# Optimization experiments

Measured on AMD Instinct MI355X. Metric: run time of the kernel, lower is better.

Reference implementation:

```python
import jax, jax.numpy as jnp
import numpy as np

N, C, H, W = 64, 128, 32, 32
EPS = 1e-5


def _layernorm_chw(x, w, b):
    # LayerNorm over normalized_shape=(C,H,W): last 3 dims
    mu = jnp.mean(x, axis=(1, 2, 3), keepdims=True)
    var = jnp.var(x, axis=(1, 2, 3), keepdims=True)
    return (x - mu) * jax.lax.rsqrt(var + EPS) * w[None] + b[None]


def _conv1x1(x, w, b):
    # x: [N,C,H,W], w: [Cout,Cin], b: [Cout]
    return jnp.einsum('oc,nchw->nohw', w, x) + b[None, :, None, None]


def setup_inputs() -> dict:
    key = jax.random.key(0)
    ks = jax.random.split(key, 12)
    d = {
        'query': jax.random.normal(ks[0], (N, C, H, W), jnp.float32),
        'key': jax.random.normal(ks[1], (N, C, H, W), jnp.float32),
        'value': jax.random.normal(ks[2], (N, C, H, W), jnp.float32),
        'ln1_w': jnp.ones((C, H, W), jnp.float32),
        'ln1_b': jnp.zeros((C, H, W), jnp.float32),
        'ln2_w': jnp.ones((C, H, W), jnp.float32),
        'ln2_b': jnp.zeros((C, H, W), jnp.float32),
        'ln3_w': jnp.ones((C, H, W), jnp.float32),
        'ln3_b': jnp.zeros((C, H, W), jnp.float32),
        'wq': jax.random.normal(ks[3], (C, C), jnp.float32) / np.sqrt(C),
        'bq': jnp.zeros((C,), jnp.float32),
        'wk': jax.random.normal(ks[4], (C, C), jnp.float32) / np.sqrt(C),
        'bk': jnp.zeros((C,), jnp.float32),
        'wv': jax.random.normal(ks[5], (C, C), jnp.float32) / np.sqrt(C),
        'bv': jnp.zeros((C,), jnp.float32),
    }
    return d


def reference(query, key, value, ln1_w, ln1_b, ln2_w, ln2_b, ln3_w, ln3_b,
              wq, bq, wk, bk, wv, bv):
    qn = _layernorm_chw(query, ln1_w, ln1_b)  # residual uses normalized query
    kn = _layernorm_chw(key, ln2_w, ln2_b)
    vn = _layernorm_chw(value, ln3_w, ln3_b)
    q = _conv1x1(qn, wq, bq).reshape(N, C, H * W)
    k = _conv1x1(kn, wk, bk).reshape(N, C, H * W)
    v = _conv1x1(vn, wv, bv).reshape(N, C, H * W)
    # attention[n,i,j] = sum_c k[n,c,i] q[n,c,j] / sqrt(C); softmax over i (dim=1)
    attn = jnp.einsum('nci,ncj->nij', k, q) / jnp.sqrt(jnp.float32(C))
    attn = jax.nn.softmax(attn, axis=1)
    out = jnp.einsum('nci,nij->ncj', v, attn).reshape(N, C, H, W)
    x = qn + out
    return x.reshape(N, -1)  # flatten(start_dim=1)
```

## Files before the change

kernel.cpp:

```cpp
#include <hip/hip_runtime.h>


#define NS 64
#define CD 128
#define SD 1024
#define MEL (CD*SD)
#define SCALE 0.08838834764831845f

typedef __attribute__((ext_vector_type(4))) float floatx4;
typedef __attribute__((ext_vector_type(8))) short short8;
typedef __attribute__((ext_vector_type(4))) short short4v;

typedef __attribute__((address_space(1))) const void global_cvoid;
typedef __attribute__((address_space(3))) void lds_void;

__device__ __forceinline__ void gl16(const void* g, void* l) {
  __builtin_amdgcn_global_load_lds((global_cvoid*)g, (lds_void*)l, 16, 0, 0);
}
__device__ __forceinline__ unsigned short f2bf(float f) {
  union { float f; unsigned int i; } v; v.f = f;
  unsigned int i = v.i;
  return (unsigned short)((i + 0x7fffu + ((i >> 16) & 1u)) >> 16);
}
__device__ __forceinline__ short8 ld8_bf16(const float* __restrict__ p) {
  floatx4 a = *(const floatx4*)p;
  floatx4 b = *(const floatx4*)(p + 4);
  short8 r;
  r[0] = (short)f2bf(a[0]); r[1] = (short)f2bf(a[1]);
  r[2] = (short)f2bf(a[2]); r[3] = (short)f2bf(a[3]);
  r[4] = (short)f2bf(b[0]); r[5] = (short)f2bf(b[1]);
  r[6] = (short)f2bf(b[2]); r[7] = (short)f2bf(b[3]);
  return r;
}
__device__ __forceinline__ floatx4 mfma16(short8 a, short8 b, floatx4 c) {
  return __builtin_amdgcn_mfma_f32_16x16x32_bf16(a, b, c, 0, 0, 0);
}

__global__ __launch_bounds__(512) void stats_kernel(
    const float* __restrict__ q, const float* __restrict__ k,
    const float* __restrict__ v, float* __restrict__ sums)
{
  int tn = blockIdx.x;
  int t = tn >> 6;
  const float* x = (t == 0 ? q : (t == 1 ? k : v)) + (size_t)(tn & 63) * MEL;
  float s1 = 0.f, s2 = 0.f;
  for (int it = 0; it < 64; ++it) {
    floatx4 u = *(const floatx4*)(x + it * 2048 + threadIdx.x * 4);
#pragma unroll
    for (int j = 0; j < 4; ++j) { float f = u[j]; s1 += f; s2 += f * f; }
  }
#pragma unroll
  for (int off = 32; off; off >>= 1) {
    s1 += __shfl_xor(s1, off, 64);
    s2 += __shfl_xor(s2, off, 64);
  }
  __shared__ float r1[8], r2[8];
  int w = threadIdx.x >> 6;
  if ((threadIdx.x & 63) == 0) { r1[w] = s1; r2[w] = s2; }
  __syncthreads();
  if (threadIdx.x == 0) {
    float a = 0.f, b = 0.f;
#pragma unroll
    for (int i = 0; i < 8; ++i) { a += r1[i]; b += r2[i]; }
    sums[tn] = a; sums[192 + tn] = b;
  }
}

__global__ __launch_bounds__(512, 4) void proj_kernel(
  const float* __restrict__ k, const float* __restrict__ v,
  const float* __restrict__ l2w, const float* __restrict__ l2b,
  const float* __restrict__ l3w, const float* __restrict__ l3b,
  const float* __restrict__ wk, const float* __restrict__ bk,
  const float* __restrict__ wv, const float* __restrict__ bv,
  const float* __restrict__ sums,
  unsigned short* __restrict__ kT, unsigned short* __restrict__ vN)
{
  int n  = blockIdx.x, t = blockIdx.y, st = blockIdx.z;
  const float* x  = (t == 0 ? k : v) + (size_t)n * MEL;
  const float* lw = (t == 0 ? l2w : l3w);
  const float* lb = (t == 0 ? l2b : l3b);
  const float* W  = (t == 0 ? wk : wv);
  const float* Bs = (t == 0 ? bk : bv);

  float mu  = sums[(t + 1) * 64 + n] * (1.f / MEL);
  float var = sums[192 + (t + 1) * 64 + n] * (1.f / MEL) - mu * mu;
  float rs  = rsqrtf(var + 1e-5f);
  float a_ln = rs, b_ln = -mu * rs;

  __shared__ __align__(16) unsigned short Xt[128 * 136];

  int tid = threadIdx.x;
  int cb = tid & 15, sb = (tid >> 4) & 15, half = tid >> 8;
  int s0 = st * 128;

  unsigned int w32[8][2];
#pragma unroll
  for (int pr = 0; pr < 2; ++pr) {
    int c0 = cb * 8 + half * 4 + pr * 2;
    const float* xp0 = x  + (size_t)c0 * SD + s0 + sb * 8;
    const float* wp0 = lw + (size_t)c0 * SD + s0 + sb * 8;
    const float* bp0 = lb + (size_t)c0 * SD + s0 + sb * 8;
    float xv0[8], xv1[8], wv0[8], wv1[8], bv0[8], bv1[8];
    *(floatx4*)xv0 = *(const floatx4*)xp0;       *(floatx4*)(xv0+4) = *(const floatx4*)(xp0+4);
    *(floatx4*)xv1 = *(const floatx4*)(xp0+SD);  *(floatx4*)(xv1+4) = *(const floatx4*)(xp0+SD+4);
    *(floatx4*)wv0 = *(const floatx4*)wp0;       *(floatx4*)(wv0+4) = *(const floatx4*)(wp0+4);
    *(floatx4*)wv1 = *(const floatx4*)(wp0+SD);  *(floatx4*)(wv1+4) = *(const floatx4*)(wp0+SD+4);
    *(floatx4*)bv0 = *(const floatx4*)bp0;       *(floatx4*)(bv0+4) = *(const floatx4*)(bp0+4);
    *(floatx4*)bv1 = *(const floatx4*)(bp0+SD);  *(floatx4*)(bv1+4) = *(const floatx4*)(bp0+SD+4);
#pragma unroll
    for (int js = 0; js < 8; ++js) {
      unsigned int lo = f2bf((xv0[js] * a_ln + b_ln) * wv0[js] + bv0[js]);
      unsigned int hi = f2bf((xv1[js] * a_ln + b_ln) * wv1[js] + bv1[js]);
      w32[js][pr] = lo | (hi << 16);
    }
  }
#pragma unroll
  for (int js = 0; js < 8; ++js) {
    unsigned int* d = (unsigned int*)&Xt[(sb * 8 + js) * 136 + cb * 8 + half * 4];
    d[0] = w32[js][0]; d[1] = w32[js][1];
  }
  __syncthreads();

  int lane = tid & 63, w = tid >> 6;
  int quad = lane >> 4, l16 = lane & 15;

  short8 Af[4];
#pragma unroll
  for (int kk = 0; kk < 4; ++kk)
    Af[kk] = ld8_bf16(W + (w * 16 + l16) * CD + kk * 32 + quad * 8);

  floatx4 acc[8];
  floatx4 zz = {0.f, 0.f, 0.f, 0.f};
#pragma unroll
  for (int nb = 0; nb < 8; ++nb) acc[nb] = zz;
#pragma unroll
  for (int kk = 0; kk < 4; ++kk)
#pragma unroll
    for (int nb = 0; nb < 8; ++nb) {
      short8 Bf = *(const short8*)&Xt[(nb * 16 + l16) * 136 + kk * 32 + quad * 8];
      acc[nb] = mfma16(Af[kk], Bf, acc[nb]);
    }

  float bsv[4];
#pragma unroll
  for (int r = 0; r < 4; ++r) bsv[r] = Bs[w * 16 + quad * 4 + r];

  if (t == 0) {
#pragma unroll
    for (int nb = 0; nb < 8; ++nb) {
      short4v pk;
#pragma unroll
      for (int r = 0; r < 4; ++r) pk[r] = (short)f2bf(acc[nb][r] + bsv[r]);
      size_t g = (size_t)n * MEL + (size_t)(s0 + nb * 16 + l16) * CD + w * 16 + quad * 4;
      *(short4v*)(kT + g) = pk;
    }
  } else {
#pragma unroll
    for (int nb = 0; nb < 8; ++nb)
#pragma unroll
      for (int r = 0; r < 4; ++r) {
        size_t g = (size_t)n * MEL + (size_t)(w * 16 + quad * 4 + r) * SD + s0 + nb * 16 + l16;
        vN[g] = f2bf(acc[nb][r] + bsv[r]);
      }
  }
}

__global__ __launch_bounds__(256, 2) void attn_kernel(
  const float* __restrict__ qraw, const float* __restrict__ l1w,
  const float* __restrict__ l1b, const float* __restrict__ wq,
  const float* __restrict__ bq,
  const unsigned short* __restrict__ kT, const unsigned short* __restrict__ vN,
  const float* __restrict__ sums, float* __restrict__ out)
{
  int n = blockIdx.x, jt = blockIdx.y;
  int j0 = jt * 128;

  __shared__ __align__(16) char smem[51712];
  unsigned short* Xt = (unsigned short*)smem;
  unsigned short* Ks = (unsigned short*)smem;
  unsigned short* Vs = (unsigned short*)(smem + 16384);
  unsigned short* Ps = (unsigned short*)(smem + 34816);
  float* l_s = (float*)(smem + 51200);

  int tid = threadIdx.x, lane = tid & 63, w = tid >> 6;
  int quad = lane >> 4, l16 = lane & 15;

  float mu  = sums[n] * (1.f / MEL);
  float var = sums[192 + n] * (1.f / MEL) - mu * mu;
  float rsd = rsqrtf(var + 1e-5f);
  float a_ln = rsd, b_ln = -mu * rsd;
  const float* qb = qraw + (size_t)n * MEL;

  {
    int cb = tid & 15, sb = tid >> 4;
    unsigned int w32[8][4];
#pragma unroll
    for (int pr = 0; pr < 4; ++pr) {
      int c0 = cb * 8 + pr * 2;
      const float* xp0 = qb  + (size_t)c0 * SD + j0 + sb * 8;
      const float* wp0 = l1w + (size_t)c0 * SD + j0 + sb * 8;
      const float* bp0 = l1b + (size_t)c0 * SD + j0 + sb * 8;
      float xv0[8], xv1[8], wv0[8], wv1[8], bv0[8], bv1[8];
      *(floatx4*)xv0 = *(const floatx4*)xp0;       *(floatx4*)(xv0+4) = *(const floatx4*)(xp0+4);
      *(floatx4*)xv1 = *(const floatx4*)(xp0+SD);  *(floatx4*)(xv1+4) = *(const floatx4*)(xp0+SD+4);
      *(floatx4*)wv0 = *(const floatx4*)wp0;       *(floatx4*)(wv0+4) = *(const floatx4*)(wp0+4);
      *(floatx4*)wv1 = *(const floatx4*)(wp0+SD);  *(floatx4*)(wv1+4) = *(const floatx4*)(wp0+SD+4);
      *(floatx4*)bv0 = *(const floatx4*)bp0;       *(floatx4*)(bv0+4) = *(const floatx4*)(bp0+4);
      *(floatx4*)bv1 = *(const floatx4*)(bp0+SD);  *(floatx4*)(bv1+4) = *(const floatx4*)(bp0+SD+4);
#pragma unroll
      for (int js = 0; js < 8; ++js) {
        unsigned int lo = f2bf((xv0[js] * a_ln + b_ln) * wv0[js] + bv0[js]);
        unsigned int hi = f2bf((xv1[js] * a_ln + b_ln) * wv1[js] + bv1[js]);
        w32[js][pr] = lo | (hi << 16);
      }
    }
#pragma unroll
    for (int js = 0; js < 8; ++js)
      *(floatx4*)&Xt[(sb * 8 + js) * 136 + cb * 8] = *(floatx4*)w32[js];
  }
  __syncthreads();

  floatx4 zz = {0.f, 0.f, 0.f, 0.f};
  {
    short8 Af[2][4];
#pragma unroll
    for (int mi = 0; mi < 2; ++mi)
#pragma unroll
      for (int kk = 0; kk < 4; ++kk)
        Af[mi][kk] = ld8_bf16(wq + ((w * 2 + mi) * 16 + l16) * CD + kk * 32 + quad * 8);
    floatx4 accq[2][8];
#pragma unroll
    for (int mi = 0; mi < 2; ++mi)
#pragma unroll
      for (int nb = 0; nb < 8; ++nb) accq[mi][nb] = zz;
#pragma unroll
    for (int kk = 0; kk < 4; ++kk)
#pragma unroll
      for (int nb = 0; nb < 8; ++nb) {
        short8 Bf = *(const short8*)&Xt[(nb * 16 + l16) * 136 + kk * 32 + quad * 8];
        accq[0][nb] = mfma16(Af[0][kk], Bf, accq[0][nb]);
        accq[1][nb] = mfma16(Af[1][kk], Bf, accq[1][nb]);
      }
    __syncthreads();
    float bqs[2][4];
#pragma unroll
    for (int mi = 0; mi < 2; ++mi)
#pragma unroll
      for (int r = 0; r < 4; ++r) bqs[mi][r] = bq[(w * 2 + mi) * 16 + quad * 4 + r];
#pragma unroll
    for (int mi = 0; mi < 2; ++mi)
#pragma unroll
      for (int nb = 0; nb < 8; ++nb) {
        short4v pk;
#pragma unroll
        for (int r = 0; r < 4; ++r) pk[r] = (short)f2bf(accq[mi][nb][r] + bqs[mi][r]);
        *(short4v*)&Xt[(nb * 16 + l16) * 136 + (w * 2 + mi) * 16 + quad * 4] = pk;
      }
  }
  __syncthreads();

  short8 Qf[2][4];
#pragma unroll
  for (int nt = 0; nt < 2; ++nt)
#pragma unroll
    for (int kk = 0; kk < 4; ++kk)
      Qf[nt][kk] = *(const short8*)&Xt[((w * 2 + nt) * 16 + l16) * 136 + kk * 32 + quad * 8];
  __syncthreads();

  floatx4 Oc[2][8];
#pragma unroll
  for (int mi = 0; mi < 2; ++mi)
#pragma unroll
    for (int nb = 0; nb < 8; ++nb) Oc[mi][nb] = zz;
  float lsum[2] = {0.f, 0.f};

  const unsigned short* kbase0 = kT + (size_t)n * MEL;
  const unsigned short* vbase0 = vN + (size_t)n * MEL;

  for (int itile = 0; itile < 16; ++itile) {
    int i0 = itile * 64;
    const unsigned short* kbase = kbase0 + (size_t)i0 * CD;
#pragma unroll
    for (int it = 0; it < 4; ++it) {
      int nch = w * 256 + it * 64 + lane;
      int i = nch >> 4, cc = nch & 15;
      int csrc = (cc & 8) | ((cc & 7) ^ (i & 7));
      gl16(kbase + i * CD + csrc * 8, (char*)Ks + (w * 256 + it * 64) * 16);
    }
#pragma unroll
    for (int it = 0; it < 4; ++it) {
      int nch = w * 256 + it * 64 + lane;
      int c = nch >> 3, ci = nch & 7;
      int isrc = ci ^ (c & 7);
      gl16(vbase0 + (size_t)c * SD + i0 + isrc * 8, (char*)Vs + (w * 256 + it * 64) * 16);
    }
    __syncthreads();

    floatx4 Sa[4][2];
#pragma unroll
    for (int mt = 0; mt < 4; ++mt) { Sa[mt][0] = zz; Sa[mt][1] = zz; }
#pragma unroll
    for (int kk = 0; kk < 4; ++kk)
#pragma unroll
      for (int mt = 0; mt < 4; ++mt) {
        short8 Kf = *(const short8*)&Ks[(mt * 16 + l16) * 128 + (((kk * 4 + quad) ^ (l16 & 7)) * 8)];
        Sa[mt][0] = mfma16(Kf, Qf[0][kk], Sa[mt][0]);
        Sa[mt][1] = mfma16(Kf, Qf[1][kk], Sa[mt][1]);
      }

#pragma unroll
    for (int nt = 0; nt < 2; ++nt) {
      int jrow = (w * 2 + nt) * 16 + l16;
      int rowbase = jrow * 64;
      int sub = (quad & 1) * 4;
#pragma unroll
      for (int mt = 0; mt < 4; ++mt) {
        float p0 = __expf(Sa[mt][nt][0] * SCALE);
        float p1 = __expf(Sa[mt][nt][1] * SCALE);
        float p2 = __expf(Sa[mt][nt][2] * SCALE);
        float p3 = __expf(Sa[mt][nt][3] * SCALE);
        lsum[nt] += (p0 + p1) + (p2 + p3);
        short4v pk;
        pk[0] = (short)f2bf(p0); pk[1] = (short)f2bf(p1);
        pk[2] = (short)f2bf(p2); pk[3] = (short)f2bf(p3);
        int ci = mt * 2 + (quad >> 1);
        int cis = ci ^ (l16 & 7);
        *(short4v*)&Ps[rowbase + cis * 8 + sub] = pk;
      }
    }
    __syncthreads();

#pragma unroll
    for (int kk = 0; kk < 2; ++kk) {
      short8 Vf[2];
#pragma unroll
      for (int mi = 0; mi < 2; ++mi) {
        int c = (w * 2 + mi) * 16 + l16;
        Vf[mi] = *(const short8*)&Vs[c * 64 + (((kk * 4 + quad) ^ (l16 & 7)) * 8)];
      }
#pragma unroll
      for (int nb = 0; nb < 8; ++nb) {
        short8 Pf = *(const short8*)&Ps[(nb * 16 + l16) * 64 + (((kk * 4 + quad) ^ (l16 & 7)) * 8)];
        Oc[0][nb] = mfma16(Vf[0], Pf, Oc[0][nb]);
        Oc[1][nb] = mfma16(Vf[1], Pf, Oc[1][nb]);
      }
    }
    __syncthreads();
  }

#pragma unroll
  for (int nt = 0; nt < 2; ++nt) {
    lsum[nt] += __shfl_xor(lsum[nt], 16, 64);
    lsum[nt] += __shfl_xor(lsum[nt], 32, 64);
  }
  if (lane < 16) { l_s[(w * 2) * 16 + l16] = lsum[0]; l_s[(w * 2 + 1) * 16 + l16] = lsum[1]; }
  __syncthreads();

  float linv[8];
#pragma unroll
  for (int nb = 0; nb < 8; ++nb) linv[nb] = 1.f / l_s[nb * 16 + l16];
#pragma unroll
  for (int mi = 0; mi < 2; ++mi) {
#pragma unroll
    for (int r = 0; r < 4; ++r) {
      int c = (w * 2 + mi) * 16 + quad * 4 + r;
      const float* qp = qb  + (size_t)c * SD + j0;
      const float* wp = l1w + (size_t)c * SD + j0;
      const float* bp = l1b + (size_t)c * SD + j0;
      float* op = out + (size_t)n * MEL + (size_t)c * SD + j0;
#pragma unroll
      for (int nb = 0; nb < 8; ++nb) {
        int j = nb * 16 + l16;
        float qn = (qp[j] * a_ln + b_ln) * wp[j] + bp[j];
        op[j] = Oc[mi][nb][r] * linv[nb] + qn;
      }
    }
  }
}

extern "C" void kernel_launch(void* const* d_in, const int* in_sizes, int n_in,
                              void* d_out, int out_size, void* d_ws, size_t ws_size,
                              hipStream_t stream)
{
  const float* q   = (const float*)d_in[0];
  const float* k   = (const float*)d_in[1];
  const float* v   = (const float*)d_in[2];
  const float* l1w = (const float*)d_in[3];
  const float* l1b = (const float*)d_in[4];
  const float* l2w = (const float*)d_in[5];
  const float* l2b = (const float*)d_in[6];
  const float* l3w = (const float*)d_in[7];
  const float* l3b = (const float*)d_in[8];
  const float* wq  = (const float*)d_in[9];
  const float* bq  = (const float*)d_in[10];
  const float* wk  = (const float*)d_in[11];
  const float* bk  = (const float*)d_in[12];
  const float* wv  = (const float*)d_in[13];
  const float* bv  = (const float*)d_in[14];

  char* ws = (char*)d_ws;
  float* sums = (float*)ws;
  unsigned short* kT = (unsigned short*)(ws + 4096);
  unsigned short* vN = kT + (size_t)NS * MEL;

  stats_kernel<<<192, 512, 0, stream>>>(q, k, v, sums);
  proj_kernel<<<dim3(64, 2, 8), 512, 0, stream>>>(k, v, l2w, l2b, l3w, l3b,
      wk, bk, wv, bv, sums, kT, vN);
  attn_kernel<<<dim3(64, 8), 256, 0, stream>>>(q, l1w, l1b, wq, bq, kT, vN,
      sums, (float*)d_out);
}
```

Measured before the change: 253.6 us.

## Split stats reduction, stage projection outputs in LDS, widen attention blocks to 512 threads

The stats kernel now splits each sample's reduction into two halves across a second grid dimension, doubling the block count. The projection kernel switches to XOR-swizzled LDS without padding and stages K/V outputs in LDS so they can be written as coalesced 16-byte stores, where V previously used scattered 2-byte stores. The attention kernel goes from 256 to 512 threads with a smaller LDS footprint, splits S and O tiles across more waves, and reuses the K buffer for P. The cost is extra syncs and combining partial softmax sums through LDS.

```diff
diff --git a/kernel.cpp b/kernel.cpp
--- a/kernel.cpp
+++ b/kernel.cpp
@@ -41,10 +41,12 @@
     const float* __restrict__ v, float* __restrict__ sums)
 {
   int tn = blockIdx.x;
+  int part = blockIdx.y;
   int t = tn >> 6;
-  const float* x = (t == 0 ? q : (t == 1 ? k : v)) + (size_t)(tn & 63) * MEL;
+  const float* x = (t == 0 ? q : (t == 1 ? k : v)) + (size_t)(tn & 63) * MEL
+                   + part * (MEL / 2);
   float s1 = 0.f, s2 = 0.f;
-  for (int it = 0; it < 64; ++it) {
+  for (int it = 0; it < 32; ++it) {
     floatx4 u = *(const floatx4*)(x + it * 2048 + threadIdx.x * 4);
 #pragma unroll
     for (int j = 0; j < 4; ++j) { float f = u[j]; s1 += f; s2 += f * f; }
@@ -62,7 +64,7 @@
     float a = 0.f, b = 0.f;
 #pragma unroll
     for (int i = 0; i < 8; ++i) { a += r1[i]; b += r2[i]; }
-    sums[tn] = a; sums[192 + tn] = b;
+    sums[part * 192 + tn] = a; sums[384 + part * 192 + tn] = b;
   }
 }
 
@@ -82,12 +84,15 @@
   const float* W  = (t == 0 ? wk : wv);
   const float* Bs = (t == 0 ? bk : bv);
 
-  float mu  = sums[(t + 1) * 64 + n] * (1.f / MEL);
-  float var = sums[192 + (t + 1) * 64 + n] * (1.f / MEL) - mu * mu;
+  int si = (t + 1) * 64 + n;
+  float s1 = sums[si] + sums[192 + si];
+  float s2 = sums[384 + si] + sums[576 + si];
+  float mu  = s1 * (1.f / MEL);
+  float var = s2 * (1.f / MEL) - mu * mu;
   float rs  = rsqrtf(var + 1e-5f);
   float a_ln = rs, b_ln = -mu * rs;
 
-  __shared__ __align__(16) unsigned short Xt[128 * 136];
+  __shared__ __align__(16) unsigned short Xt[128 * 128];
 
   int tid = threadIdx.x;
   int cb = tid & 15, sb = (tid >> 4) & 15, half = tid >> 8;
@@ -116,7 +121,7 @@
   }
 #pragma unroll
   for (int js = 0; js < 8; ++js) {
-    unsigned int* d = (unsigned int*)&Xt[(sb * 8 + js) * 136 + cb * 8 + half * 4];
+    unsigned int* d = (unsigned int*)&Xt[(sb * 8 + js) * 128 + ((cb ^ js) * 8) + half * 4];
     d[0] = w32[js][0]; d[1] = w32[js][1];
   }
   __syncthreads();
@@ -124,48 +129,67 @@
   int lane = tid & 63, w = tid >> 6;
   int quad = lane >> 4, l16 = lane & 15;
 
-  short8 Af[4];
+  short8 Wf[4];
 #pragma unroll
   for (int kk = 0; kk < 4; ++kk)
-    Af[kk] = ld8_bf16(W + (w * 16 + l16) * CD + kk * 32 + quad * 8);
+    Wf[kk] = ld8_bf16(W + (w * 16 + l16) * CD + kk * 32 + quad * 8);
 
   floatx4 acc[8];
   floatx4 zz = {0.f, 0.f, 0.f, 0.f};
 #pragma unroll
-  for (int nb = 0; nb < 8; ++nb) acc[nb] = zz;
+  for (int sblk = 0; sblk < 8; ++sblk) acc[sblk] = zz;
 #pragma unroll
   for (int kk = 0; kk < 4; ++kk)
 #pragma unroll
-    for (int nb = 0; nb < 8; ++nb) {
-      short8 Bf = *(const short8*)&Xt[(nb * 16 + l16) * 136 + kk * 32 + quad * 8];
-      acc[nb] = mfma16(Af[kk], Bf, acc[nb]);
-    }
-
-  float bsv[4];
-#pragma unroll
-  for (int r = 0; r < 4; ++r) bsv[r] = Bs[w * 16 + quad * 4 + r];
+    for (int sblk = 0; sblk < 8; ++sblk) {
+      short8 Xf = *(const short8*)&Xt[(sblk * 16 + l16) * 128 +
+                                      (((kk * 4 + quad) ^ (l16 & 7)) * 8)];
+      acc[sblk] = (t == 0) ? mfma16(Wf[kk], Xf, acc[sblk])
+                           : mfma16(Xf, Wf[kk], acc[sblk]);
+    }
+  __syncthreads();
 
   if (t == 0) {
-#pragma unroll
-    for (int nb = 0; nb < 8; ++nb) {
+    float bsv[4];
+#pragma unroll
+    for (int r = 0; r < 4; ++r) bsv[r] = Bs[w * 16 + quad * 4 + r];
+#pragma unroll
+    for (int sblk = 0; sblk < 8; ++sblk) {
       short4v pk;
 #pragma unroll
-      for (int r = 0; r < 4; ++r) pk[r] = (short)f2bf(acc[nb][r] + bsv[r]);
-      size_t g = (size_t)n * MEL + (size_t)(s0 + nb * 16 + l16) * CD + w * 16 + quad * 4;
-      *(short4v*)(kT + g) = pk;
+      for (int r = 0; r < 4; ++r) pk[r] = (short)f2bf(acc[sblk][r] + bsv[r]);
+      int row = sblk * 16 + l16;
+      int cblk = w * 2 + (quad >> 1);
+      *(short4v*)&Xt[row * 128 + ((cblk ^ (l16 & 7)) * 8) + (quad & 1) * 4] = pk;
     }
   } else {
-#pragma unroll
-    for (int nb = 0; nb < 8; ++nb)
-#pragma unroll
-      for (int r = 0; r < 4; ++r) {
-        size_t g = (size_t)n * MEL + (size_t)(w * 16 + quad * 4 + r) * SD + s0 + nb * 16 + l16;
-        vN[g] = f2bf(acc[nb][r] + bsv[r]);
-      }
-  }
-}
-
-__global__ __launch_bounds__(256, 2) void attn_kernel(
+    float bsv = Bs[w * 16 + l16];
+#pragma unroll
+    for (int sblk = 0; sblk < 8; ++sblk) {
+      short4v pk;
+#pragma unroll
+      for (int r = 0; r < 4; ++r) pk[r] = (short)f2bf(acc[sblk][r] + bsv);
+      int row = w * 16 + l16;
+      int cblk = sblk * 2 + (quad >> 1);
+      *(short4v*)&Xt[row * 128 + ((cblk ^ (l16 & 7)) * 8) + (quad & 1) * 4] = pk;
+    }
+  }
+  __syncthreads();
+
+  unsigned short* outp = (t == 0 ? kT : vN);
+#pragma unroll
+  for (int it = 0; it < 4; ++it) {
+    int id = it * 512 + tid;
+    int row = id >> 4, ch = id & 15;
+    short8 u = *(const short8*)&Xt[row * 128 + ((ch ^ (row & 7)) * 8)];
+    size_t g;
+    if (t == 0) g = (size_t)n * MEL + (size_t)(s0 + row) * CD + ch * 8;
+    else        g = (size_t)n * MEL + (size_t)row * SD + s0 + ch * 8;
+    *(short8*)(outp + g) = u;
+  }
+}
+
+__global__ __launch_bounds__(512, 4) void attn_kernel(
   const float* __restrict__ qraw, const float* __restrict__ l1w,
   const float* __restrict__ l1b, const float* __restrict__ wq,
   const float* __restrict__ bq,
@@ -175,28 +199,30 @@
   int n = blockIdx.x, jt = blockIdx.y;
   int j0 = jt * 128;
 
-  __shared__ __align__(16) char smem[51712];
+  __shared__ __align__(16) char smem[33792];
   unsigned short* Xt = (unsigned short*)smem;
   unsigned short* Ks = (unsigned short*)smem;
+  unsigned short* Ps = (unsigned short*)smem;
   unsigned short* Vs = (unsigned short*)(smem + 16384);
-  unsigned short* Ps = (unsigned short*)(smem + 34816);
-  float* l_s = (float*)(smem + 51200);
+  float* l_part = (float*)(smem + 32768);
 
   int tid = threadIdx.x, lane = tid & 63, w = tid >> 6;
   int quad = lane >> 4, l16 = lane & 15;
 
-  float mu  = sums[n] * (1.f / MEL);
-  float var = sums[192 + n] * (1.f / MEL) - mu * mu;
+  float s1 = sums[n] + sums[192 + n];
+  float s2 = sums[384 + n] + sums[576 + n];
+  float mu  = s1 * (1.f / MEL);
+  float var = s2 * (1.f / MEL) - mu * mu;
   float rsd = rsqrtf(var + 1e-5f);
   float a_ln = rsd, b_ln = -mu * rsd;
   const float* qb = qraw + (size_t)n * MEL;
 
   {
-    int cb = tid & 15, sb = tid >> 4;
-    unsigned int w32[8][4];
-#pragma unroll
-    for (int pr = 0; pr < 4; ++pr) {
-      int c0 = cb * 8 + pr * 2;
+    int cb = tid & 15, sb = (tid >> 4) & 15, half = tid >> 8;
+    unsigned int w32[8][2];
+#pragma unroll
+    for (int pr = 0; pr < 2; ++pr) {
+      int c0 = cb * 8 + half * 4 + pr * 2;
       const float* xp0 = qb  + (size_t)c0 * SD + j0 + sb * 8;
       const float* wp0 = l1w + (size_t)c0 * SD + j0 + sb * 8;
       const float* bp0 = l1b + (size_t)c0 * SD + j0 + sb * 8;
@@ -215,63 +241,61 @@
       }
     }
 #pragma unroll
-    for (int js = 0; js < 8; ++js)
-      *(floatx4*)&Xt[(sb * 8 + js) * 136 + cb * 8] = *(floatx4*)w32[js];
+    for (int js = 0; js < 8; ++js) {
+      unsigned int* d = (unsigned int*)&Xt[(sb * 8 + js) * 128 + ((cb ^ js) * 8) + half * 4];
+      d[0] = w32[js][0]; d[1] = w32[js][1];
+    }
   }
   __syncthreads();
 
   floatx4 zz = {0.f, 0.f, 0.f, 0.f};
   {
-    short8 Af[2][4];
-#pragma unroll
-    for (int mi = 0; mi < 2; ++mi)
-#pragma unroll
-      for (int kk = 0; kk < 4; ++kk)
-        Af[mi][kk] = ld8_bf16(wq + ((w * 2 + mi) * 16 + l16) * CD + kk * 32 + quad * 8);
-    floatx4 accq[2][8];
-#pragma unroll
-    for (int mi = 0; mi < 2; ++mi)
-#pragma unroll
-      for (int nb = 0; nb < 8; ++nb) accq[mi][nb] = zz;
+    short8 Wf[4];
 #pragma unroll
     for (int kk = 0; kk < 4; ++kk)
+      Wf[kk] = ld8_bf16(wq + (w * 16 + l16) * CD + kk * 32 + quad * 8);
+    floatx4 accq[8];
+#pragma unroll
+    for (int nb = 0; nb < 8; ++nb) accq[nb] = zz;
+#pragma unroll
+    for (int kk = 0; kk < 4; ++kk)
 #pragma unroll
       for (int nb = 0; nb < 8; ++nb) {
-        short8 Bf = *(const short8*)&Xt[(nb * 16 + l16) * 136 + kk * 32 + quad * 8];
-        accq[0][nb] = mfma16(Af[0][kk], Bf, accq[0][nb]);
-        accq[1][nb] = mfma16(Af[1][kk], Bf, accq[1][nb]);
+        short8 Bf = *(const short8*)&Xt[(nb * 16 + l16) * 128 +
+                                        (((kk * 4 + quad) ^ (l16 & 7)) * 8)];
+        accq[nb] = mfma16(Wf[kk], Bf, accq[nb]);
       }
     __syncthreads();
-    float bqs[2][4];
-#pragma unroll
-    for (int mi = 0; mi < 2; ++mi)
-#pragma unroll
-      for (int r = 0; r < 4; ++r) bqs[mi][r] = bq[(w * 2 + mi) * 16 + quad * 4 + r];
-#pragma unroll
-    for (int mi = 0; mi < 2; ++mi)
-#pragma unroll
-      for (int nb = 0; nb < 8; ++nb) {
-        short4v pk;
-#pragma unroll
-        for (int r = 0; r < 4; ++r) pk[r] = (short)f2bf(accq[mi][nb][r] + bqs[mi][r]);
-        *(short4v*)&Xt[(nb * 16 + l16) * 136 + (w * 2 + mi) * 16 + quad * 4] = pk;
-      }
+    float bqs[4];
+#pragma unroll
+    for (int r = 0; r < 4; ++r) bqs[r] = bq[w * 16 + quad * 4 + r];
+#pragma unroll
+    for (int nb = 0; nb < 8; ++nb) {
+      short4v pk;
+#pragma unroll
+      for (int r = 0; r < 4; ++r) pk[r] = (short)f2bf(accq[nb][r] + bqs[r]);
+      int row = nb * 16 + l16;
+      int cblk = w * 2 + (quad >> 1);
+      *(short4v*)&Xt[row * 128 + ((cblk ^ (l16 & 7)) * 8) + (quad & 1) * 4] = pk;
+    }
   }
   __syncthreads();
 
   short8 Qf[2][4];
 #pragma unroll
-  for (int nt = 0; nt < 2; ++nt)
+  for (int ntl = 0; ntl < 2; ++ntl) {
+    int row = ((w >> 1) * 2 + ntl) * 16 + l16;
 #pragma unroll
     for (int kk = 0; kk < 4; ++kk)
-      Qf[nt][kk] = *(const short8*)&Xt[((w * 2 + nt) * 16 + l16) * 136 + kk * 32 + quad * 8];
-  __syncthreads();
-
-  floatx4 Oc[2][8];
+      Qf[ntl][kk] = *(const short8*)&Xt[row * 128 + (((kk * 4 + quad) ^ (l16 & 7)) * 8)];
+  }
+  __syncthreads();
+
+  floatx4 Oc[2][4];
 #pragma unroll
   for (int mi = 0; mi < 2; ++mi)
 #pragma unroll
-    for (int nb = 0; nb < 8; ++nb) Oc[mi][nb] = zz;
+    for (int nb = 0; nb < 4; ++nb) Oc[mi][nb] = zz;
   float lsum[2] = {0.f, 0.f};
 
   const unsigned short* kbase0 = kT + (size_t)n * MEL;
@@ -281,51 +305,56 @@
     int i0 = itile * 64;
     const unsigned short* kbase = kbase0 + (size_t)i0 * CD;
 #pragma unroll
-    for (int it = 0; it < 4; ++it) {
-      int nch = w * 256 + it * 64 + lane;
+    for (int it = 0; it < 2; ++it) {
+      int nch = it * 512 + tid;
       int i = nch >> 4, cc = nch & 15;
       int csrc = (cc & 8) | ((cc & 7) ^ (i & 7));
-      gl16(kbase + i * CD + csrc * 8, (char*)Ks + (w * 256 + it * 64) * 16);
-    }
-#pragma unroll
-    for (int it = 0; it < 4; ++it) {
-      int nch = w * 256 + it * 64 + lane;
+      gl16(kbase + i * CD + csrc * 8, Ks + nch * 8);
+    }
+#pragma unroll
+    for (int it = 0; it < 2; ++it) {
+      int nch = it * 512 + tid;
       int c = nch >> 3, ci = nch & 7;
       int isrc = ci ^ (c & 7);
-      gl16(vbase0 + (size_t)c * SD + i0 + isrc * 8, (char*)Vs + (w * 256 + it * 64) * 16);
+      gl16(vbase0 + (size_t)c * SD + i0 + isrc * 8, Vs + nch * 8);
     }
     __syncthreads();
 
-    floatx4 Sa[4][2];
-#pragma unroll
-    for (int mt = 0; mt < 4; ++mt) { Sa[mt][0] = zz; Sa[mt][1] = zz; }
-#pragma unroll
-    for (int kk = 0; kk < 4; ++kk)
-#pragma unroll
-      for (int mt = 0; mt < 4; ++mt) {
-        short8 Kf = *(const short8*)&Ks[(mt * 16 + l16) * 128 + (((kk * 4 + quad) ^ (l16 & 7)) * 8)];
-        Sa[mt][0] = mfma16(Kf, Qf[0][kk], Sa[mt][0]);
-        Sa[mt][1] = mfma16(Kf, Qf[1][kk], Sa[mt][1]);
-      }
-
-#pragma unroll
-    for (int nt = 0; nt < 2; ++nt) {
-      int jrow = (w * 2 + nt) * 16 + l16;
-      int rowbase = jrow * 64;
-      int sub = (quad & 1) * 4;
-#pragma unroll
-      for (int mt = 0; mt < 4; ++mt) {
-        float p0 = __expf(Sa[mt][nt][0] * SCALE);
-        float p1 = __expf(Sa[mt][nt][1] * SCALE);
-        float p2 = __expf(Sa[mt][nt][2] * SCALE);
-        float p3 = __expf(Sa[mt][nt][3] * SCALE);
-        lsum[nt] += (p0 + p1) + (p2 + p3);
+    floatx4 Sa[2][2];
+#pragma unroll
+    for (int a = 0; a < 2; ++a) { Sa[a][0] = zz; Sa[a][1] = zz; }
+#pragma unroll
+    for (int kk = 0; kk < 4; ++kk) {
+      short8 Kf[2];
+#pragma unroll
+      for (int mtl = 0; mtl < 2; ++mtl) {
+        int row = ((w & 1) * 2 + mtl) * 16 + l16;
+        Kf[mtl] = *(const short8*)&Ks[row * 128 + (((kk * 4 + quad) ^ (l16 & 7)) * 8)];
+      }
+#pragma unroll
+      for (int mtl = 0; mtl < 2; ++mtl)
+#pragma unroll
+        for (int ntl = 0; ntl < 2; ++ntl)
+          Sa[mtl][ntl] = mfma16(Kf[mtl], Qf[ntl][kk], Sa[mtl][ntl]);
+    }
+    __syncthreads();
+
+#pragma unroll
+    for (int mtl = 0; mtl < 2; ++mtl) {
+      int mt = (w & 1) * 2 + mtl;
+#pragma unroll
+      for (int ntl = 0; ntl < 2; ++ntl) {
+        float p0 = __expf(Sa[mtl][ntl][0] * SCALE);
+        float p1 = __expf(Sa[mtl][ntl][1] * SCALE);
+        float p2 = __expf(Sa[mtl][ntl][2] * SCALE);
+        float p3 = __expf(Sa[mtl][ntl][3] * SCALE);
+        lsum[ntl] += (p0 + p1) + (p2 + p3);
         short4v pk;
         pk[0] = (short)f2bf(p0); pk[1] = (short)f2bf(p1);
         pk[2] = (short)f2bf(p2); pk[3] = (short)f2bf(p3);
-        int ci = mt * 2 + (quad >> 1);
-        int cis = ci ^ (l16 & 7);
-        *(short4v*)&Ps[rowbase + cis * 8 + sub] = pk;
+        int jrow = ((w >> 1) * 2 + ntl) * 16 + l16;
+        int cis = (mt * 2 + (quad >> 1)) ^ (l16 & 7);
+        *(short4v*)&Ps[jrow * 64 + cis * 8 + (quad & 1) * 4] = pk;
       }
     }
     __syncthreads();
@@ -335,12 +364,13 @@
       short8 Vf[2];
 #pragma unroll
       for (int mi = 0; mi < 2; ++mi) {
-        int c = (w * 2 + mi) * 16 + l16;
+        int c = ((w & 3) * 2 + mi) * 16 + l16;
         Vf[mi] = *(const short8*)&Vs[c * 64 + (((kk * 4 + quad) ^ (l16 & 7)) * 8)];
       }
 #pragma unroll
-      for (int nb = 0; nb < 8; ++nb) {
-        short8 Pf = *(const short8*)&Ps[(nb * 16 + l16) * 64 + (((kk * 4 + quad) ^ (l16 & 7)) * 8)];
+      for (int nb = 0; nb < 4; ++nb) {
+        int j = ((w >> 2) * 4 + nb) * 16 + l16;
+        short8 Pf = *(const short8*)&Ps[j * 64 + (((kk * 4 + quad) ^ (l16 & 7)) * 8)];
         Oc[0][nb] = mfma16(Vf[0], Pf, Oc[0][nb]);
         Oc[1][nb] = mfma16(Vf[1], Pf, Oc[1][nb]);
       }
@@ -349,28 +379,35 @@
   }
 
 #pragma unroll
-  for (int nt = 0; nt < 2; ++nt) {
-    lsum[nt] += __shfl_xor(lsum[nt], 16, 64);
-    lsum[nt] += __shfl_xor(lsum[nt], 32, 64);
-  }
-  if (lane < 16) { l_s[(w * 2) * 16 + l16] = lsum[0]; l_s[(w * 2 + 1) * 16 + l16] = lsum[1]; }
-  __syncthreads();
-
-  float linv[8];
-#pragma unroll
-  for (int nb = 0; nb < 8; ++nb) linv[nb] = 1.f / l_s[nb * 16 + l16];
+  for (int ntl = 0; ntl < 2; ++ntl) {
+    lsum[ntl] += __shfl_xor(lsum[ntl], 16, 64);
+    lsum[ntl] += __shfl_xor(lsum[ntl], 32, 64);
+  }
+  if (lane < 16) {
+#pragma unroll
+    for (int ntl = 0; ntl < 2; ++ntl)
+      l_part[(w & 1) * 128 + ((w >> 1) * 2 + ntl) * 16 + lane] = lsum[ntl];
+  }
+  __syncthreads();
+
+  float linv[4];
+#pragma unroll
+  for (int nb = 0; nb < 4; ++nb) {
+    int j = ((w >> 2) * 4 + nb) * 16 + l16;
+    linv[nb] = 1.f / (l_part[j] + l_part[128 + j]);
+  }
 #pragma unroll
   for (int mi = 0; mi < 2; ++mi) {
 #pragma unroll
     for (int r = 0; r < 4; ++r) {
-      int c = (w * 2 + mi) * 16 + quad * 4 + r;
+      int c = ((w & 3) * 2 + mi) * 16 + quad * 4 + r;
       const float* qp = qb  + (size_t)c * SD + j0;
       const float* wp = l1w + (size_t)c * SD + j0;
       const float* bp = l1b + (size_t)c * SD + j0;
       float* op = out + (size_t)n * MEL + (size_t)c * SD + j0;
 #pragma unroll
-      for (int nb = 0; nb < 8; ++nb) {
-        int j = nb * 16 + l16;
+      for (int nb = 0; nb < 4; ++nb) {
+        int j = ((w >> 2) * 4 + nb) * 16 + l16;
         float qn = (qp[j] * a_ln + b_ln) * wp[j] + bp[j];
         op[j] = Oc[mi][nb][r] * linv[nb] + qn;
       }
@@ -403,9 +440,9 @@
   unsigned short* kT = (unsigned short*)(ws + 4096);
   unsigned short* vN = kT + (size_t)NS * MEL;
 
-  stats_kernel<<<192, 512, 0, stream>>>(q, k, v, sums);
+  stats_kernel<<<dim3(192, 2), 512, 0, stream>>>(q, k, v, sums);
   proj_kernel<<<dim3(64, 2, 8), 512, 0, stream>>>(k, v, l2w, l2b, l3w, l3b,
       wk, bk, wv, bv, sums, kT, vN);
-  attn_kernel<<<dim3(64, 8), 256, 0, stream>>>(q, l1w, l1b, wq, bq, kT, vN,
+  attn_kernel<<<dim3(64, 8), 512, 0, stream>>>(q, l1w, l1b, wq, bq, kT, vN,
       sums, (float*)d_out);
 }
```

Result: no change. 258.4 us (+1.9%).
